# Kernel tuning notes

Hardware: AMD Instinct MI355X
Metric: run time of the kernel (lower is better)

## Reference

```python
import jax, jax.numpy as jnp
import numpy as np

HID = 2048      # hidden_size
NH = 32         # num_heads
G = 8           # num_kv_groups
R = NH // G     # repeat factor (heads per kv group)
HD = HID // NH  # head_dim = 64
SCALE = HD ** 0.5


def setup_inputs() -> dict:
    key = jax.random.key(0)
    ks = jax.random.split(key, 10)
    B, S = 2, 1024
    x = jax.random.normal(ks[0], (B, S, HID), dtype=jnp.float32)
    attention_mask = jnp.ones((B, S, S), dtype=jnp.float32)
    # Linear params stored as [in, out] (y = x @ W + b), same math as torch Linear.
    Wq = jax.random.normal(ks[1], (HID, HID), dtype=jnp.float32) * 0.02
    bq = jnp.zeros((HID,), dtype=jnp.float32)
    Wk = jax.random.normal(ks[2], (HID, G * HD), dtype=jnp.float32) * 0.02
    bk = jnp.zeros((G * HD,), dtype=jnp.float32)
    Wv = jax.random.normal(ks[3], (HID, G * HD), dtype=jnp.float32) * 0.02
    bv = jnp.zeros((G * HD,), dtype=jnp.float32)
    Wo = jax.random.normal(ks[4], (HID, HID), dtype=jnp.float32) * 0.02
    bo = jnp.zeros((HID,), dtype=jnp.float32)
    return {"x": x, "attention_mask": attention_mask,
            "Wq": Wq, "bq": bq, "Wk": Wk, "bk": bk,
            "Wv": Wv, "bv": bv, "Wo": Wo, "bo": bo}


def reference(x, attention_mask, Wq, bq, Wk, bk, Wv, bv, Wo, bo):
    B, S, _ = x.shape
    # Projections. Group heads as (G, R) instead of repeat_interleave:
    # repeat_interleave(key, R, dim=2) duplicates each kv group R times, which is
    # exactly sharing key[:, :, g] across the R heads of group g.
    q = (x @ Wq + bq).reshape(B, S, G, R, HD)   # [B,S,G,R,HD] (heads = G*R in order)
    k = (x @ Wk + bk).reshape(B, S, G, HD)      # [B,S,G,HD]
    v = (x @ Wv + bv).reshape(B, S, G, HD)
    # scores [B,G,R,Sq,Sk] == torch's [B, NH, Sq, Sk] with NH = G*R
    scores = jnp.einsum('bqgrd,bkgd->bgrqk', q, k) / SCALE
    scores = scores * attention_mask[:, None, None]  # multiplicative mask per head
    w = jax.nn.softmax(scores, axis=-1)
    out = jnp.einsum('bgrqk,bkgd->bqgrd', w, v).reshape(B, S, HID)
    return out @ Wo + bo + x
```

## Files before the change

kernel.cpp:

```cpp
#include <hip/hip_runtime.h>

typedef unsigned short u16;
typedef unsigned int u32;
typedef __attribute__((ext_vector_type(8))) short bf16x8;
typedef __attribute__((ext_vector_type(4))) float f32x4;

#define HID 2048
#define S_LEN 1024
#define BATCH 2
#define G_KV 8
#define R_REP 4
#define HD 64
#define NQKV 3072

__device__ __forceinline__ u16 f2bf(float f) {
    union { u32 u; float ff; } x; x.ff = f;
    u32 u = x.u;
    u += 0x7FFFu + ((u >> 16) & 1u);
    return (u16)(u >> 16);
}

__device__ __forceinline__ void gload_lds16(const void* g, void* l) {
    __builtin_amdgcn_global_load_lds((const __attribute__((address_space(1))) void*)g,
                                     (__attribute__((address_space(3))) void*)l,
                                     16, 0, 0);
}

__global__ __launch_bounds__(256) void prep(const float* __restrict__ x,
                                            const float* __restrict__ Wq,
                                            const float* __restrict__ Wk,
                                            const float* __restrict__ Wv,
                                            const float* __restrict__ Wo,
                                            u16* __restrict__ Xb,
                                            u16* __restrict__ WqkvT,
                                            u16* __restrict__ WoT) {
    __shared__ float tile[32][33];
    int bid = blockIdx.x, tid = threadIdx.x;

    if (bid < 2048) {
        int i = (bid * 256 + tid) * 8;
        float4 a = *(const float4*)(x + i);
        float4 b = *(const float4*)(x + i + 4);
        u16 t[8] = {f2bf(a.x), f2bf(a.y), f2bf(a.z), f2bf(a.w),
                    f2bf(b.x), f2bf(b.y), f2bf(b.z), f2bf(b.w)};
        *(uint4*)(Xb + i) = *(const uint4*)t;
        return;
    }

    int tx = tid & 31, ty = tid >> 5;
    if (bid < 8192) {
        int local = bid - 2048;
        int n0 = (local % 96) * 32, k0 = (local / 96) * 32;
        const float* in; int N, nc0;
        if (n0 < 2048)      { in = Wq; N = 2048; nc0 = n0; }
        else if (n0 < 2560) { in = Wk; N = 512;  nc0 = n0 - 2048; }
        else                { in = Wv; N = 512;  nc0 = n0 - 2560; }
#pragma unroll
        for (int j = 0; j < 4; ++j)
            tile[ty + j * 8][tx] = in[(size_t)(k0 + ty + j * 8) * N + nc0 + tx];
        __syncthreads();
#pragma unroll
        for (int j = 0; j < 4; ++j)
            WqkvT[(size_t)(n0 + ty + j * 8) * 2048 + k0 + tx] = f2bf(tile[tx][ty + j * 8]);
        return;
    }

    {
        int local = bid - 8192;
        int n0 = (local & 63) * 32, k0 = (local >> 6) * 32;
#pragma unroll
        for (int j = 0; j < 4; ++j)
            tile[ty + j * 8][tx] = Wo[(size_t)(k0 + ty + j * 8) * 2048 + n0 + tx];
        __syncthreads();
#pragma unroll
        for (int j = 0; j < 4; ++j)
            WoT[(size_t)(n0 + ty + j * 8) * 2048 + k0 + tx] = f2bf(tile[tx][ty + j * 8]);
    }
}

__global__ __launch_bounds__(256) void gemm_qkv(const u16* __restrict__ Xb,
                                                const u16* __restrict__ WT,
                                                const float* __restrict__ bq,
                                                const float* __restrict__ bk,
                                                const float* __restrict__ bv,
                                                u16* __restrict__ qb,
                                                u16* __restrict__ kb,
                                                u16* __restrict__ vb) {
    __shared__ __align__(16) u16 As[2][64 * 32];
    __shared__ __align__(16) u16 Bs[2][128 * 32];
    int tid = threadIdx.x;
    int w = tid >> 6, lane = tid & 63, quad = lane >> 4, l16 = lane & 15;
    int m0 = blockIdx.y * 64, n0 = blockIdx.x * 128;
    int wr = (w >> 1) * 32, wc = (w & 1) * 64;
    int srow = lane >> 2, scol = (lane & 3) * 8;

    const u16* aP  = &Xb[(size_t)(m0 + w * 16 + srow) * 2048 + scol];
    const u16* bP0 = &WT[(size_t)(n0 + w * 32 + srow) * 2048 + scol];
    const u16* bP1 = &WT[(size_t)(n0 + w * 32 + 16 + srow) * 2048 + scol];

    f32x4 acc[2][4];
#pragma unroll
    for (int i = 0; i < 2; ++i)
#pragma unroll
        for (int j = 0; j < 4; ++j) acc[i][j] = (f32x4){0.f, 0.f, 0.f, 0.f};

    gload_lds16(aP,  &As[0][(w * 16) * 32]);
    gload_lds16(bP0, &Bs[0][(w * 32) * 32]);
    gload_lds16(bP1, &Bs[0][(w * 32 + 16) * 32]);
    __syncthreads();

    int cur = 0;
    for (int k0 = 0; k0 < 2048; k0 += 32) {
        int kn = k0 + 32;
        if (kn < 2048) {
            gload_lds16(aP + kn,  &As[cur ^ 1][(w * 16) * 32]);
            gload_lds16(bP0 + kn, &Bs[cur ^ 1][(w * 32) * 32]);
            gload_lds16(bP1 + kn, &Bs[cur ^ 1][(w * 32 + 16) * 32]);
        }
        bf16x8 af[2], bfr[4];
#pragma unroll
        for (int mt = 0; mt < 2; ++mt)
            af[mt] = *(const bf16x8*)&As[cur][(wr + mt * 16 + l16) * 32 + quad * 8];
#pragma unroll
        for (int nt = 0; nt < 4; ++nt)
            bfr[nt] = *(const bf16x8*)&Bs[cur][(wc + nt * 16 + l16) * 32 + quad * 8];
#pragma unroll
        for (int mt = 0; mt < 2; ++mt)
#pragma unroll
            for (int nt = 0; nt < 4; ++nt)
                acc[mt][nt] = __builtin_amdgcn_mfma_f32_16x16x32_bf16(af[mt], bfr[nt], acc[mt][nt], 0, 0, 0);
        __syncthreads();
        cur ^= 1;
    }

#pragma unroll
    for (int nt = 0; nt < 4; ++nt) {
        int n = n0 + wc + nt * 16 + l16;
        float bias;
        if (n < 2048) bias = bq[n];
        else if (n < 2560) bias = bk[n - 2048];
        else bias = bv[n - 2560];
#pragma unroll
        for (int mt = 0; mt < 2; ++mt) {
#pragma unroll
            for (int reg = 0; reg < 4; ++reg) {
                int m = m0 + wr + mt * 16 + quad * 4 + reg;
                float val = acc[mt][nt][reg] + bias;
                int b = m >> 10, s = m & 1023;
                if (n < 2048) {
                    int g = n >> 8, r = (n >> 6) & 3, d = n & 63;
                    qb[((((size_t)(b * G_KV + g) * R_REP + r) * S_LEN) + s) * HD + d] = f2bf(val * 0.125f);
                } else if (n < 2560) {
                    int n2 = n - 2048, g = n2 >> 6, d = n2 & 63;
                    kb[(((size_t)(b * G_KV + g) * S_LEN) + s) * HD + d] = f2bf(val);
                } else {
                    int n2 = n - 2560, g = n2 >> 6, d = n2 & 63;
                    vb[(((size_t)(b * G_KV + g) * HD + d) * S_LEN) + s] = f2bf(val);
                }
            }
        }
    }
}

__global__ __launch_bounds__(256) void attn_mfma(const u16* __restrict__ qbuf,
                                                 const u16* __restrict__ kbuf,
                                                 const u16* __restrict__ vtbuf,
                                                 const float* __restrict__ mask,
                                                 u16* __restrict__ aout) {
    __shared__ __align__(16) u16 Ks[64 * 72];
    __shared__ __align__(16) u16 Vs[64 * 72];
    __shared__ __align__(16) u16 Ps[64 * 72];
    __shared__ __align__(16) float Ms[16 * 68];
    __shared__ float l_lds[64];

    int d = blockIdx.x;
    int qblk = d & 63, g = (d >> 6) & 7, b = d >> 9;
    int s0 = qblk * 16;

    int tid = threadIdx.x;
    int w = tid >> 6, lane = tid & 63, quad = lane >> 4, l16 = lane & 15;
    int qs = w * 16 + l16;

    const u16* qrow = qbuf +
        ((((size_t)(b * G_KV + g) * R_REP + w) * S_LEN) + s0 + l16) * HD;
    bf16x8 qf0 = *(const bf16x8*)(qrow + quad * 8);
    bf16x8 qf1 = *(const bf16x8*)(qrow + 32 + quad * 8);

    f32x4 o_acc[4];
#pragma unroll
    for (int i = 0; i < 4; ++i) o_acc[i] = (f32x4){0.f, 0.f, 0.f, 0.f};
    float l_part = 0.f;

    const u16* kbase  = kbuf  + (size_t)(b * G_KV + g) * S_LEN * HD;
    const u16* vtbase = vtbuf + (size_t)(b * G_KV + g) * HD * S_LEN;
    const float* mstage = mask + ((size_t)b * S_LEN + s0 + (tid >> 4)) * S_LEN + (tid & 15) * 4;
    int msrow = tid >> 4, mscol = (tid & 15) * 4;

    int srow = tid >> 2, sc = (tid & 3) * 16;

    uint4 kp0, kp1, vp0, vp1;
    f32x4 mp;
    {
        const u16* kr = kbase + (size_t)srow * HD + sc;
        kp0 = *(const uint4*)kr; kp1 = *(const uint4*)(kr + 8);
        const u16* vr = vtbase + (size_t)srow * S_LEN + sc;
        vp0 = *(const uint4*)vr; vp1 = *(const uint4*)(vr + 8);
        mp = *(const f32x4*)mstage;
    }

    for (int kt = 0; kt < 16; ++kt) {
        __syncthreads();
        *(uint4*)&Ks[srow * 72 + sc]     = kp0;
        *(uint4*)&Ks[srow * 72 + sc + 8] = kp1;
        *(uint4*)&Vs[srow * 72 + sc]     = vp0;
        *(uint4*)&Vs[srow * 72 + sc + 8] = vp1;
        *(f32x4*)&Ms[msrow * 68 + mscol] = mp;
        __syncthreads();

        if (kt < 15) {
            int nk = (kt + 1) * 64;
            const u16* kr = kbase + (size_t)(nk + srow) * HD + sc;
            kp0 = *(const uint4*)kr; kp1 = *(const uint4*)(kr + 8);
            const u16* vr = vtbase + (size_t)srow * S_LEN + nk + sc;
            vp0 = *(const uint4*)vr; vp1 = *(const uint4*)(vr + 8);
            mp = *(const f32x4*)(mstage + nk);
        }

#pragma unroll
        for (int mt = 0; mt < 4; ++mt) {
            bf16x8 af0 = *(const bf16x8*)&Ks[(mt * 16 + l16) * 72 + quad * 8];
            bf16x8 af1 = *(const bf16x8*)&Ks[(mt * 16 + l16) * 72 + 32 + quad * 8];
            f32x4 z = (f32x4){0.f, 0.f, 0.f, 0.f};
            z = __builtin_amdgcn_mfma_f32_16x16x32_bf16(af0, qf0, z, 0, 0, 0);
            f32x4 s = __builtin_amdgcn_mfma_f32_16x16x32_bf16(af1, qf1, s = z, 0, 0, 0);

            f32x4 mv = *(const f32x4*)&Ms[l16 * 68 + mt * 16 + quad * 4];

            u32 er[4];
#pragma unroll
            for (int rg = 0; rg < 4; ++rg) {
                float e = __expf(s[rg] * mv[rg]);
                u32 u = __float_as_uint(e) + 0x8000u;
                er[rg] = u;
                l_part += __uint_as_float(u & 0xFFFF0000u);
            }
            uint2 pk;
            pk.x = __builtin_amdgcn_perm(er[1], er[0], 0x07060302u);
            pk.y = __builtin_amdgcn_perm(er[3], er[2], 0x07060302u);
            *(uint2*)&Ps[qs * 72 + mt * 16 + quad * 4] = pk;
        }

        bf16x8 pf0 = *(const bf16x8*)&Ps[qs * 72 + quad * 8];
        bf16x8 pf1 = *(const bf16x8*)&Ps[qs * 72 + 32 + quad * 8];
#pragma unroll
        for (int nt = 0; nt < 4; ++nt) {
            bf16x8 vf0 = *(const bf16x8*)&Vs[(nt * 16 + l16) * 72 + quad * 8];
            bf16x8 vf1 = *(const bf16x8*)&Vs[(nt * 16 + l16) * 72 + 32 + quad * 8];
            o_acc[nt] = __builtin_amdgcn_mfma_f32_16x16x32_bf16(pf0, vf0, o_acc[nt], 0, 0, 0);
            o_acc[nt] = __builtin_amdgcn_mfma_f32_16x16x32_bf16(pf1, vf1, o_acc[nt], 0, 0, 0);
        }
    }

    l_part += __shfl_xor(l_part, 16);
    l_part += __shfl_xor(l_part, 32);
    l_lds[w * 16 + l16] = l_part;

#pragma unroll
    for (int reg = 0; reg < 4; ++reg) {
        int qloc = quad * 4 + reg;
        float inv = 1.0f / l_lds[w * 16 + qloc];
        u16* dst = aout + ((size_t)(b * S_LEN + s0 + qloc)) * HID + (g * R_REP + w) * HD;
#pragma unroll
        for (int nt = 0; nt < 4; ++nt)
            dst[nt * 16 + l16] = f2bf(o_acc[nt][reg] * inv);
    }
}

__global__ __launch_bounds__(256) void gemm_o(const u16* __restrict__ A,
                                              const u16* __restrict__ WT,
                                              const float* __restrict__ bo,
                                              const float* __restrict__ Xres,
                                              float* __restrict__ out) {
    __shared__ __align__(16) u16 As[2][64 * 32];
    __shared__ __align__(16) u16 Bs[2][128 * 32];
    int tid = threadIdx.x;
    int w = tid >> 6, lane = tid & 63, quad = lane >> 4, l16 = lane & 15;
    int m0 = blockIdx.y * 64, n0 = blockIdx.x * 128;
    int wr = (w >> 1) * 32, wc = (w & 1) * 64;
    int srow = lane >> 2, scol = (lane & 3) * 8;

    const u16* aP  = &A[(size_t)(m0 + w * 16 + srow) * 2048 + scol];
    const u16* bP0 = &WT[(size_t)(n0 + w * 32 + srow) * 2048 + scol];
    const u16* bP1 = &WT[(size_t)(n0 + w * 32 + 16 + srow) * 2048 + scol];

    f32x4 acc[2][4];
#pragma unroll
    for (int i = 0; i < 2; ++i)
#pragma unroll
        for (int j = 0; j < 4; ++j) acc[i][j] = (f32x4){0.f, 0.f, 0.f, 0.f};

    gload_lds16(aP,  &As[0][(w * 16) * 32]);
    gload_lds16(bP0, &Bs[0][(w * 32) * 32]);
    gload_lds16(bP1, &Bs[0][(w * 32 + 16) * 32]);
    __syncthreads();

    int cur = 0;
    for (int k0 = 0; k0 < 2048; k0 += 32) {
        int kn = k0 + 32;
        if (kn < 2048) {
            gload_lds16(aP + kn,  &As[cur ^ 1][(w * 16) * 32]);
            gload_lds16(bP0 + kn, &Bs[cur ^ 1][(w * 32) * 32]);
            gload_lds16(bP1 + kn, &Bs[cur ^ 1][(w * 32 + 16) * 32]);
        }
        bf16x8 af[2], bfr[4];
#pragma unroll
        for (int mt = 0; mt < 2; ++mt)
            af[mt] = *(const bf16x8*)&As[cur][(wr + mt * 16 + l16) * 32 + quad * 8];
#pragma unroll
        for (int nt = 0; nt < 4; ++nt)
            bfr[nt] = *(const bf16x8*)&Bs[cur][(wc + nt * 16 + l16) * 32 + quad * 8];
#pragma unroll
        for (int mt = 0; mt < 2; ++mt)
#pragma unroll
            for (int nt = 0; nt < 4; ++nt)
                acc[mt][nt] = __builtin_amdgcn_mfma_f32_16x16x32_bf16(af[mt], bfr[nt], acc[mt][nt], 0, 0, 0);
        __syncthreads();
        cur ^= 1;
    }

#pragma unroll
    for (int nt = 0; nt < 4; ++nt) {
        int n = n0 + wc + nt * 16 + l16;
        float bias = bo[n];
#pragma unroll
        for (int mt = 0; mt < 2; ++mt) {
#pragma unroll
            for (int reg = 0; reg < 4; ++reg) {
                int m = m0 + wr + mt * 16 + quad * 4 + reg;
                out[(size_t)m * 2048 + n] = acc[mt][nt][reg] + bias + Xres[(size_t)m * 2048 + n];
            }
        }
    }
}

extern "C" void kernel_launch(void* const* d_in, const int* in_sizes, int n_in,
                              void* d_out, int out_size, void* d_ws, size_t ws_size,
                              hipStream_t stream) {
    const float* x    = (const float*)d_in[0];
    const float* mask = (const float*)d_in[1];
    const float* Wq   = (const float*)d_in[2];
    const float* bq   = (const float*)d_in[3];
    const float* Wk   = (const float*)d_in[4];
    const float* bk   = (const float*)d_in[5];
    const float* Wv   = (const float*)d_in[6];
    const float* bv   = (const float*)d_in[7];
    const float* Wo   = (const float*)d_in[8];
    const float* bo   = (const float*)d_in[9];
    float* out = (float*)d_out;

    u16* ws = (u16*)d_ws;
    size_t off = 0;
    u16* WqkvT = ws + off; off += (size_t)NQKV * 2048;
    u16* WoT   = ws + off; off += (size_t)2048 * 2048;
    u16* q_buf = ws + off; off += (size_t)BATCH * G_KV * R_REP * S_LEN * HD;
    u16* k_buf = ws + off; off += (size_t)BATCH * G_KV * S_LEN * HD;
    u16* v_buf = ws + off; off += (size_t)BATCH * G_KV * S_LEN * HD;
    u16* a_out = ws + off; off += (size_t)2048 * 2048;
    u16* Xb    = a_out;

    prep<<<dim3(12288), 256, 0, stream>>>(x, Wq, Wk, Wv, Wo, Xb, WqkvT, WoT);

    gemm_qkv<<<dim3(NQKV / 128, 2048 / 64), 256, 0, stream>>>(Xb, WqkvT, bq, bk, bv,
                                                              q_buf, k_buf, v_buf);

    attn_mfma<<<dim3(BATCH * G_KV * 64), 256, 0, stream>>>(
        q_buf, k_buf, v_buf, mask, a_out);

    gemm_o<<<dim3(2048 / 128, 2048 / 64), 256, 0, stream>>>(a_out, WoT, bo, x, out);
}
```

Before: 235.5 us.

## Process 32 query rows per attention block to reuse staged K/V tiles

New measurement: 232.6 us. Within noise of the previous version (-1.2%).

```diff
diff --git a/kernel.cpp b/kernel.cpp
--- a/kernel.cpp
+++ b/kernel.cpp
@@ -169,13 +169,13 @@
                                                  u16* __restrict__ aout) {
     __shared__ __align__(16) u16 Ks[64 * 72];
     __shared__ __align__(16) u16 Vs[64 * 72];
-    __shared__ __align__(16) u16 Ps[64 * 72];
-    __shared__ __align__(16) float Ms[16 * 68];
-    __shared__ float l_lds[64];
+    __shared__ __align__(16) u16 Ps[2][64 * 72];
+    __shared__ __align__(16) float Ms[32 * 68];
+    __shared__ float l_lds[128];
 
     int d = blockIdx.x;
-    int qblk = d & 63, g = (d >> 6) & 7, b = d >> 9;
-    int s0 = qblk * 16;
+    int qblk = d & 31, g = (d >> 5) & 7, b = d >> 8;
+    int s0 = qblk * 32;
 
     int tid = threadIdx.x;
     int w = tid >> 6, lane = tid & 63, quad = lane >> 4, l16 = lane & 15;
@@ -183,29 +183,34 @@
 
     const u16* qrow = qbuf +
         ((((size_t)(b * G_KV + g) * R_REP + w) * S_LEN) + s0 + l16) * HD;
-    bf16x8 qf0 = *(const bf16x8*)(qrow + quad * 8);
-    bf16x8 qf1 = *(const bf16x8*)(qrow + 32 + quad * 8);
-
-    f32x4 o_acc[4];
-#pragma unroll
-    for (int i = 0; i < 4; ++i) o_acc[i] = (f32x4){0.f, 0.f, 0.f, 0.f};
-    float l_part = 0.f;
+    bf16x8 qf0_lo = *(const bf16x8*)(qrow + quad * 8);
+    bf16x8 qf1_lo = *(const bf16x8*)(qrow + 32 + quad * 8);
+    bf16x8 qf0_hi = *(const bf16x8*)(qrow + 16 * HD + quad * 8);
+    bf16x8 qf1_hi = *(const bf16x8*)(qrow + 16 * HD + 32 + quad * 8);
+
+    f32x4 o_lo[4], o_hi[4];
+#pragma unroll
+    for (int i = 0; i < 4; ++i) {
+        o_lo[i] = (f32x4){0.f, 0.f, 0.f, 0.f};
+        o_hi[i] = (f32x4){0.f, 0.f, 0.f, 0.f};
+    }
+    float l_lo = 0.f, l_hi = 0.f;
 
     const u16* kbase  = kbuf  + (size_t)(b * G_KV + g) * S_LEN * HD;
     const u16* vtbase = vtbuf + (size_t)(b * G_KV + g) * HD * S_LEN;
-    const float* mstage = mask + ((size_t)b * S_LEN + s0 + (tid >> 4)) * S_LEN + (tid & 15) * 4;
-    int msrow = tid >> 4, mscol = (tid & 15) * 4;
+    int msrow = tid >> 3, mscol = (tid & 7) * 8;
+    const float* mstage = mask + ((size_t)b * S_LEN + s0 + msrow) * S_LEN + mscol;
 
     int srow = tid >> 2, sc = (tid & 3) * 16;
 
     uint4 kp0, kp1, vp0, vp1;
-    f32x4 mp;
+    f32x4 mp0, mp1;
     {
         const u16* kr = kbase + (size_t)srow * HD + sc;
         kp0 = *(const uint4*)kr; kp1 = *(const uint4*)(kr + 8);
         const u16* vr = vtbase + (size_t)srow * S_LEN + sc;
         vp0 = *(const uint4*)vr; vp1 = *(const uint4*)(vr + 8);
-        mp = *(const f32x4*)mstage;
+        mp0 = *(const f32x4*)mstage; mp1 = *(const f32x4*)(mstage + 4);
     }
 
     for (int kt = 0; kt < 16; ++kt) {
@@ -214,7 +219,8 @@
         *(uint4*)&Ks[srow * 72 + sc + 8] = kp1;
         *(uint4*)&Vs[srow * 72 + sc]     = vp0;
         *(uint4*)&Vs[srow * 72 + sc + 8] = vp1;
-        *(f32x4*)&Ms[msrow * 68 + mscol] = mp;
+        *(f32x4*)&Ms[msrow * 68 + mscol]     = mp0;
+        *(f32x4*)&Ms[msrow * 68 + mscol + 4] = mp1;
         __syncthreads();
 
         if (kt < 15) {
@@ -223,56 +229,83 @@
             kp0 = *(const uint4*)kr; kp1 = *(const uint4*)(kr + 8);
             const u16* vr = vtbase + (size_t)srow * S_LEN + nk + sc;
             vp0 = *(const uint4*)vr; vp1 = *(const uint4*)(vr + 8);
-            mp = *(const f32x4*)(mstage + nk);
+            mp0 = *(const f32x4*)(mstage + nk);
+            mp1 = *(const f32x4*)(mstage + nk + 4);
         }
 
 #pragma unroll
         for (int mt = 0; mt < 4; ++mt) {
             bf16x8 af0 = *(const bf16x8*)&Ks[(mt * 16 + l16) * 72 + quad * 8];
             bf16x8 af1 = *(const bf16x8*)&Ks[(mt * 16 + l16) * 72 + 32 + quad * 8];
-            f32x4 z = (f32x4){0.f, 0.f, 0.f, 0.f};
-            z = __builtin_amdgcn_mfma_f32_16x16x32_bf16(af0, qf0, z, 0, 0, 0);
-            f32x4 s = __builtin_amdgcn_mfma_f32_16x16x32_bf16(af1, qf1, s = z, 0, 0, 0);
-
-            f32x4 mv = *(const f32x4*)&Ms[l16 * 68 + mt * 16 + quad * 4];
+            f32x4 z0 = (f32x4){0.f, 0.f, 0.f, 0.f};
+            z0 = __builtin_amdgcn_mfma_f32_16x16x32_bf16(af0, qf0_lo, z0, 0, 0, 0);
+            f32x4 s_lo = __builtin_amdgcn_mfma_f32_16x16x32_bf16(af1, qf1_lo, z0, 0, 0, 0);
+            f32x4 z1 = (f32x4){0.f, 0.f, 0.f, 0.f};
+            z1 = __builtin_amdgcn_mfma_f32_16x16x32_bf16(af0, qf0_hi, z1, 0, 0, 0);
+            f32x4 s_hi = __builtin_amdgcn_mfma_f32_16x16x32_bf16(af1, qf1_hi, z1, 0, 0, 0);
+
+            f32x4 mv_lo = *(const f32x4*)&Ms[l16 * 68 + mt * 16 + quad * 4];
+            f32x4 mv_hi = *(const f32x4*)&Ms[(16 + l16) * 68 + mt * 16 + quad * 4];
 
             u32 er[4];
 #pragma unroll
             for (int rg = 0; rg < 4; ++rg) {
-                float e = __expf(s[rg] * mv[rg]);
+                float e = __expf(s_lo[rg] * mv_lo[rg]);
                 u32 u = __float_as_uint(e) + 0x8000u;
                 er[rg] = u;
-                l_part += __uint_as_float(u & 0xFFFF0000u);
+                l_lo += __uint_as_float(u & 0xFFFF0000u);
             }
             uint2 pk;
             pk.x = __builtin_amdgcn_perm(er[1], er[0], 0x07060302u);
             pk.y = __builtin_amdgcn_perm(er[3], er[2], 0x07060302u);
-            *(uint2*)&Ps[qs * 72 + mt * 16 + quad * 4] = pk;
-        }
-
-        bf16x8 pf0 = *(const bf16x8*)&Ps[qs * 72 + quad * 8];
-        bf16x8 pf1 = *(const bf16x8*)&Ps[qs * 72 + 32 + quad * 8];
+            *(uint2*)&Ps[0][qs * 72 + mt * 16 + quad * 4] = pk;
+
+#pragma unroll
+            for (int rg = 0; rg < 4; ++rg) {
+                float e = __expf(s_hi[rg] * mv_hi[rg]);
+                u32 u = __float_as_uint(e) + 0x8000u;
+                er[rg] = u;
+                l_hi += __uint_as_float(u & 0xFFFF0000u);
+            }
+            pk.x = __builtin_amdgcn_perm(er[1], er[0], 0x07060302u);
+            pk.y = __builtin_amdgcn_perm(er[3], er[2], 0x07060302u);
+            *(uint2*)&Ps[1][qs * 72 + mt * 16 + quad * 4] = pk;
+        }
+
+        bf16x8 pf0_lo = *(const bf16x8*)&Ps[0][qs * 72 + quad * 8];
+        bf16x8 pf1_lo = *(const bf16x8*)&Ps[0][qs * 72 + 32 + quad * 8];
+        bf16x8 pf0_hi = *(const bf16x8*)&Ps[1][qs * 72 + quad * 8];
+        bf16x8 pf1_hi = *(const bf16x8*)&Ps[1][qs * 72 + 32 + quad * 8];
 #pragma unroll
         for (int nt = 0; nt < 4; ++nt) {
             bf16x8 vf0 = *(const bf16x8*)&Vs[(nt * 16 + l16) * 72 + quad * 8];
             bf16x8 vf1 = *(const bf16x8*)&Vs[(nt * 16 + l16) * 72 + 32 + quad * 8];
-            o_acc[nt] = __builtin_amdgcn_mfma_f32_16x16x32_bf16(pf0, vf0, o_acc[nt], 0, 0, 0);
-            o_acc[nt] = __builtin_amdgcn_mfma_f32_16x16x32_bf16(pf1, vf1, o_acc[nt], 0, 0, 0);
-        }
-    }
-
-    l_part += __shfl_xor(l_part, 16);
-    l_part += __shfl_xor(l_part, 32);
-    l_lds[w * 16 + l16] = l_part;
+            o_lo[nt] = __builtin_amdgcn_mfma_f32_16x16x32_bf16(pf0_lo, vf0, o_lo[nt], 0, 0, 0);
+            o_lo[nt] = __builtin_amdgcn_mfma_f32_16x16x32_bf16(pf1_lo, vf1, o_lo[nt], 0, 0, 0);
+            o_hi[nt] = __builtin_amdgcn_mfma_f32_16x16x32_bf16(pf0_hi, vf0, o_hi[nt], 0, 0, 0);
+            o_hi[nt] = __builtin_amdgcn_mfma_f32_16x16x32_bf16(pf1_hi, vf1, o_hi[nt], 0, 0, 0);
+        }
+    }
+
+    l_lo += __shfl_xor(l_lo, 16);
+    l_lo += __shfl_xor(l_lo, 32);
+    l_hi += __shfl_xor(l_hi, 16);
+    l_hi += __shfl_xor(l_hi, 32);
+    l_lds[qs] = l_lo;
+    l_lds[64 + qs] = l_hi;
 
 #pragma unroll
     for (int reg = 0; reg < 4; ++reg) {
         int qloc = quad * 4 + reg;
-        float inv = 1.0f / l_lds[w * 16 + qloc];
-        u16* dst = aout + ((size_t)(b * S_LEN + s0 + qloc)) * HID + (g * R_REP + w) * HD;
-#pragma unroll
-        for (int nt = 0; nt < 4; ++nt)
-            dst[nt * 16 + l16] = f2bf(o_acc[nt][reg] * inv);
+        float inv_lo = 1.0f / l_lds[w * 16 + qloc];
+        float inv_hi = 1.0f / l_lds[64 + w * 16 + qloc];
+        u16* dst_lo = aout + ((size_t)(b * S_LEN + s0 + qloc)) * HID + (g * R_REP + w) * HD;
+        u16* dst_hi = dst_lo + (size_t)16 * HID;
+#pragma unroll
+        for (int nt = 0; nt < 4; ++nt) {
+            dst_lo[nt * 16 + l16] = f2bf(o_lo[nt][reg] * inv_lo);
+            dst_hi[nt * 16 + l16] = f2bf(o_hi[nt][reg] * inv_hi);
+        }
     }
 }
 
@@ -373,7 +406,7 @@
     gemm_qkv<<<dim3(NQKV / 128, 2048 / 64), 256, 0, stream>>>(Xb, WqkvT, bq, bk, bv,
                                                               q_buf, k_buf, v_buf);
 
-    attn_mfma<<<dim3(BATCH * G_KV * 64), 256, 0, stream>>>(
+    attn_mfma<<<dim3(BATCH * G_KV * 32), 256, 0, stream>>>(
         q_buf, k_buf, v_buf, mask, a_out);
 
     gemm_o<<<dim3(2048 / 128, 2048 / 64), 256, 0, stream>>>(a_out, WoT, bo, x, out);
```
